# Optimization experiments

Measured on AMD Instinct MI355X. Metric: run time of the kernel, lower is better.

The kernel has to match this reference:

```python
import jax, jax.numpy as jnp
import numpy as np

C = 32          # d_model / channels
D_STATE = 32
D_CONV = 4
EXPAND = 2
D_INNER = EXPAND * C          # 64
DT_RANK = (C + 15) // 16      # ceil(32/16) = 2
EPS = 1e-5


def _conv2d(x, w, b):
    # x: (B,C,H,W), w: (O,I,3,3), stride 1, padding 1 (torch Conv2d)
    y = jax.lax.conv_general_dilated(
        x, w, window_strides=(1, 1), padding=[(1, 1), (1, 1)],
        dimension_numbers=("NCHW", "OIHW", "NCHW"))
    return y + b[None, :, None, None]


def _silu(x):
    return x * jax.nn.sigmoid(x)


def _mamba(xs, in_proj_w, conv1d_w, conv1d_b, x_proj_w, dt_proj_w, dt_proj_b,
           A_log, Dp, out_proj_w):
    # xs: (B, L, C)
    xz = xs @ in_proj_w.T                       # (B, L, 2*D_INNER)
    xm, z = jnp.split(xz, 2, axis=-1)           # each (B, L, D_INNER)

    # causal depthwise conv1d along L (torch: padding=d_conv-1 then [..., :L])
    xc = xm.transpose(0, 2, 1)                  # (B, D_INNER, L)
    xc = jax.lax.conv_general_dilated(
        xc, conv1d_w, window_strides=(1,), padding=[(D_CONV - 1, 0)],
        dimension_numbers=("NCH", "OIH", "NCH"),
        feature_group_count=D_INNER)
    xm = _silu((xc + conv1d_b[None, :, None]).transpose(0, 2, 1))  # (B,L,D_INNER)

    x_dbl = xm @ x_proj_w.T                     # (B, L, DT_RANK + 2*D_STATE)
    dt = x_dbl[..., :DT_RANK]
    Bm = x_dbl[..., DT_RANK:DT_RANK + D_STATE]  # (B, L, N)
    Cm = x_dbl[..., DT_RANK + D_STATE:]         # (B, L, N)

    delta = jax.nn.softplus(dt @ dt_proj_w.T + dt_proj_b)  # (B, L, D_INNER)
    A = -jnp.exp(A_log)                                     # (D_INNER, N)

    deltaA = jnp.exp(delta[..., None] * A)                           # (B,L,D,N)
    deltaBx = delta[..., None] * Bm[:, :, None, :] * xm[..., None]   # (B,L,D,N)

    def combine(c1, c2):
        a1, b1 = c1
        a2, b2 = c2
        return a1 * a2, a2 * b1 + b2

    # parallel linear recurrence h_t = deltaA_t * h_{t-1} + deltaBx_t
    _, hstate = jax.lax.associative_scan(combine, (deltaA, deltaBx), axis=1)

    y = jnp.einsum("bldn,bln->bld", hstate, Cm) + xm * Dp
    y = y * _silu(z)
    return y @ out_proj_w.T                     # (B, L, C)


def setup_inputs() -> dict:
    key = jax.random.key(0)
    ks = jax.random.split(key, 16)
    s = 0.02
    inp = {
        "x": jax.random.normal(ks[0], (4, C, 64, 64), dtype=jnp.float32),
        "conv1_w": jax.random.normal(ks[1], (2 * C, C, 3, 3), jnp.float32) * s,
        "conv1_b": jnp.zeros((2 * C,), jnp.float32),
        "conv2_w": jax.random.normal(ks[2], (C, 2 * C, 3, 3), jnp.float32) * s,
        "conv2_b": jnp.zeros((C,), jnp.float32),
        "ln_g": jnp.ones((C,), jnp.float32),
        "ln_b": jnp.zeros((C,), jnp.float32),
        "in_proj_w": jax.random.normal(ks[3], (2 * D_INNER, C), jnp.float32) * s,
        "conv1d_w": jax.random.normal(ks[4], (D_INNER, 1, D_CONV), jnp.float32) * 0.1,
        "conv1d_b": jnp.zeros((D_INNER,), jnp.float32),
        "x_proj_w": jax.random.normal(ks[5], (DT_RANK + 2 * D_STATE, D_INNER), jnp.float32) * s,
        "dt_proj_w": jax.random.normal(ks[6], (D_INNER, DT_RANK), jnp.float32) * 0.1,
        "dt_proj_b": jax.random.normal(ks[7], (D_INNER,), jnp.float32) * 0.1 - 4.0,
        "A_log": jnp.log(jnp.tile(jnp.arange(1, D_STATE + 1, dtype=jnp.float32), (D_INNER, 1))),
        "Dp": jnp.ones((D_INNER,), jnp.float32),
        "out_proj_w": jax.random.normal(ks[8], (C, D_INNER), jnp.float32) * s,
        "smooth_w": jax.random.normal(ks[9], (C, C, 3, 3), jnp.float32) * s,
        "smooth_b": jnp.zeros((C,), jnp.float32),
    }
    return inp


def reference(x, conv1_w, conv1_b, conv2_w, conv2_b, ln_g, ln_b,
              in_proj_w, conv1d_w, conv1d_b, x_proj_w, dt_proj_w, dt_proj_b,
              A_log, Dp, out_proj_w, smooth_w, smooth_b):
    b, c, h, w = x.shape
    # convb residual
    t = jax.nn.relu(_conv2d(x, conv1_w, conv1_b))
    x = _conv2d(t, conv2_w, conv2_b) + x
    # reshape (b,c,h,w) -> (b, h*w, c) row-major (faithful to torch .reshape)
    xs = x.reshape(b, -1, c)
    # LayerNorm over last dim
    mu = jnp.mean(xs, axis=-1, keepdims=True)
    var = jnp.mean(jnp.square(xs - mu), axis=-1, keepdims=True)
    xs = (xs - mu) * jax.lax.rsqrt(var + EPS) * ln_g + ln_b
    # Mamba block
    y = _mamba(xs, in_proj_w, conv1d_w, conv1d_b, x_proj_w, dt_proj_w,
               dt_proj_b, A_log, Dp, out_proj_w)
    y = y.transpose(0, 2, 1).reshape(b, c, h, w)
    return _conv2d(y, smooth_w, smooth_b)
```

## Files before the change

kernel.cpp:

```cpp
#include <hip/hip_runtime.h>
#include <math.h>

#define SEQL 4096
#define L2E 1.44269504088896340736f

#if defined(__has_builtin)
#if __has_builtin(__builtin_amdgcn_exp2f)
#define FAST_EXP2(x) __builtin_amdgcn_exp2f(x)
#endif
#endif
#ifndef FAST_EXP2
#define FAST_EXP2(x) exp2f(x)
#endif

__device__ __forceinline__ float sigmoid_f(float x){ return 1.0f/(1.0f+expf(-x)); }

template<int CI, int CO, int COG, bool RELU, bool RES>
__global__ __launch_bounds__(256) void conv3x3_k(const float* __restrict__ in,
    const float* __restrict__ wgt, const float* __restrict__ bias,
    const float* __restrict__ res, float* __restrict__ out)
{
  constexpr int CIT = CI/4;
  __shared__ float tin[4][2][6][72];
  __shared__ float red[3][4][COG][66];
  const int tid  = threadIdx.x;
  const int lane = tid & 63;
  const int ty   = tid >> 6;
  const int h0   = blockIdx.x * 4;
  const int co0  = blockIdx.y * COG;
  const int b    = blockIdx.z;

  if (lane < 24){
    int cl = lane / 12, rem = lane % 12, r = rem >> 1, side = rem & 1;
    tin[ty][cl][r][side ? 68 : 3] = 0.0f;
  }

  float acc[4][COG];
  #pragma unroll
  for (int rr=0;rr<4;++rr)
    #pragma unroll
    for (int u=0;u<COG;++u) acc[rr][u] = 0.0f;

  const int ci0 = ty*CIT;
  for (int cig = ci0; cig < ci0 + CIT; cig += 2){
    #pragma unroll
    for (int k=0;k<3;++k){
      int idx4 = lane + (k<<6);
      int row  = idx4 >> 4;
      int cl = row/6, r = row - cl*6;
      int w4 = (idx4 & 15) << 2;
      int h  = h0 - 1 + r;
      float4 v = make_float4(0.f,0.f,0.f,0.f);
      if (h>=0 && h<64)
        v = *(const float4*)(in + ((size_t)(b*CI+cig+cl)*64 + h)*64 + w4);
      *(float4*)&tin[ty][cl][r][4+w4] = v;
    }
    #pragma unroll
    for (int cl=0; cl<2; ++cl){
      float rv[6][3];
      #pragma unroll
      for (int r=0;r<6;++r)
        #pragma unroll
        for (int c=0;c<3;++c)
          rv[r][c] = tin[ty][cl][r][3+lane+c];
      #pragma unroll
      for (int u=0;u<COG;++u){
        const float* wp = wgt + ((size_t)(co0+u)*CI + cig + cl)*9;
        #pragma unroll
        for (int rr=0;rr<4;++rr)
          #pragma unroll
          for (int j=0;j<3;++j){
            acc[rr][u] = fmaf(rv[rr+j][0], wp[3*j+0], acc[rr][u]);
            acc[rr][u] = fmaf(rv[rr+j][1], wp[3*j+1], acc[rr][u]);
            acc[rr][u] = fmaf(rv[rr+j][2], wp[3*j+2], acc[rr][u]);
          }
      }
    }
  }
  if (ty > 0){
    #pragma unroll
    for (int rr=0;rr<4;++rr)
      #pragma unroll
      for (int u=0;u<COG;++u) red[ty-1][rr][u][lane] = acc[rr][u];
  }
  __syncthreads();
  if (ty == 0){
    #pragma unroll
    for (int rr=0;rr<4;++rr)
      #pragma unroll
      for (int u=0;u<COG;++u){
        float s = acc[rr][u] + red[0][rr][u][lane] + red[1][rr][u][lane]
                + red[2][rr][u][lane] + bias[co0+u];
        size_t ob = ((size_t)(b*CO+co0+u)*64 + h0+rr)*64 + lane;
        if constexpr (RES)  s += res[ob];
        if constexpr (RELU) s = fmaxf(s, 0.0f);
        out[ob] = s;
      }
  }
}

__global__ __launch_bounds__(1024, 4) void mamba_in_k(const float* __restrict__ x2,
    const float* __restrict__ g, const float* __restrict__ be,
    const float* __restrict__ Wip, const float* __restrict__ cw,
    const float* __restrict__ cb, const float* __restrict__ Wxp,
    const float* __restrict__ Wdt, const float* __restrict__ bdt,
    const float* __restrict__ A_log,
    float* __restrict__ xm2, float* __restrict__ szb, float* __restrict__ dlt,
    float* __restrict__ Bm, float* __restrict__ Cm,
    float* __restrict__ cA, float* __restrict__ cH)
{
  __shared__ __align__(16) float xn[68][37];
  __shared__ __align__(16) float xm[64][68];
  __shared__ __align__(16) float xtT[64][68];
  __shared__ __align__(16) float xd[64][67];
  float (*xbT)[68] = reinterpret_cast<float(*)[68]>(&xn[0][0]);
  const int tid = threadIdx.x, lane = tid & 63, ty = tid >> 6;
  const int bi = blockIdx.x >> 6;
  const int l0 = (blockIdx.x & 63) << 6;

  {
    const int row = tid >> 3, sub = tid & 7;
    if (row < 67){
      const int tok = l0 - 3 + row;
      const int c0 = sub << 2;
      if (tok >= 0){
        float4 f = *(const float4*)(x2 + (size_t)bi*131072 + (size_t)tok*32 + c0);
        float s = (f.x+f.y)+(f.z+f.w);
        s += __shfl_xor(s,1); s += __shfl_xor(s,2); s += __shfl_xor(s,4);
        const float mu = s * 0.03125f;
        float dx=f.x-mu, dy=f.y-mu, dz=f.z-mu, dw=f.w-mu;
        float q = (dx*dx+dy*dy)+(dz*dz+dw*dw);
        q += __shfl_xor(q,1); q += __shfl_xor(q,2); q += __shfl_xor(q,4);
        const float rstd = 1.0f/sqrtf(q*0.03125f + 1e-5f);
        xn[row][c0+0] = dx*rstd*g[c0+0] + be[c0+0];
        xn[row][c0+1] = dy*rstd*g[c0+1] + be[c0+1];
        xn[row][c0+2] = dz*rstd*g[c0+2] + be[c0+2];
        xn[row][c0+3] = dw*rstd*g[c0+3] + be[c0+3];
      } else {
        xn[row][c0+0]=0.0f; xn[row][c0+1]=0.0f;
        xn[row][c0+2]=0.0f; xn[row][c0+3]=0.0f;
      }
    }
  }
  __syncthreads();

  if (ty < 8){
    const int d0 = ty*8;
    float xvA[32];
    #pragma unroll
    for (int c=0;c<32;++c) xvA[c] = xn[lane][c];
    #pragma unroll
    for (int jj=0;jj<8;++jj){
      const float* wr = Wip + (d0+jj)*32;
      float a = 0.0f;
      #pragma unroll
      for (int c=0;c<32;++c) a = fmaf(xvA[c], wr[c], a);
      xm[d0+jj][lane] = a;
    }
    if (lane < 3){
      float xvB[32];
      #pragma unroll
      for (int c=0;c<32;++c) xvB[c] = xn[64+lane][c];
      #pragma unroll
      for (int jj=0;jj<8;++jj){
        const float* wr = Wip + (d0+jj)*32;
        float a = 0.0f;
        #pragma unroll
        for (int c=0;c<32;++c) a = fmaf(xvB[c], wr[c], a);
        xm[d0+jj][64+lane] = a;
      }
    }
  } else {
    const int d0z = (ty-8)*8;
    float xvC[32];
    #pragma unroll
    for (int c=0;c<32;++c) xvC[c] = xn[lane+3][c];
    #pragma unroll
    for (int jj=0;jj<8;++jj){
      const float* wr = Wip + (64+d0z+jj)*32;
      float a = 0.0f;
      #pragma unroll
      for (int c=0;c<32;++c) a = fmaf(xvC[c], wr[c], a);
      szb[((size_t)(bi*64+d0z+jj))*SEQL + l0 + lane] = a * sigmoid_f(a);
    }
  }
  __syncthreads();

  #pragma unroll
  for (int jj=0;jj<4;++jj){
    int d = ty*4 + jj;
    float a = xm[d][lane]*cw[d*4] + xm[d][lane+1]*cw[d*4+1]
            + xm[d][lane+2]*cw[d*4+2] + xm[d][lane+3]*cw[d*4+3] + cb[d];
    float s = a * sigmoid_f(a);
    xtT[d][lane] = s;
    xm2[((size_t)(bi*64+d))*SEQL + l0 + lane] = s;
  }
  __syncthreads();

  {
    float xv[64];
    #pragma unroll
    for (int c=0;c<64;++c) xv[c] = xtT[c][lane];
    for (int j=ty; j<66; j+=16){
      const float* wr = Wxp + j*64;
      float a = 0.0f;
      #pragma unroll
      for (int c=0;c<64;++c) a = fmaf(xv[c], wr[c], a);
      xd[lane][j] = a;
    }
  }
  __syncthreads();

  {
    float dt0 = xd[lane][0], dt1 = xd[lane][1];
    #pragma unroll
    for (int k=0;k<4;++k){
      int d2 = ty*4 + k;
      float v = dt0*Wdt[d2*2] + dt1*Wdt[d2*2+1] + bdt[d2];
      float sp = fmaxf(v,0.0f) + log1pf(expf(-fabsf(v)));
      dlt[((size_t)(bi*64+d2))*SEQL + l0 + lane] = sp;
      xm[d2][lane] = sp;
    }
    const int which = ty >> 3, gq = ty & 7;
    float* dst = which ? Cm : Bm;
    size_t base = ((size_t)bi*SEQL + l0 + lane)*32 + gq*4;
    const int s2 = 2 + which*32;
    float4 f0;
    f0.x = xd[lane][s2+gq+ 0]; f0.y = xd[lane][s2+gq+ 8];
    f0.z = xd[lane][s2+gq+16]; f0.w = xd[lane][s2+gq+24];
    *(float4*)(dst + base) = f0;
    if (!which){
      xbT[gq     ][lane] = f0.x;
      xbT[gq +  8][lane] = f0.y;
      xbT[gq + 16][lane] = f0.z;
      xbT[gq + 24][lane] = f0.w;
    }
  }
  __syncthreads();

  {
    const int d  = tid >> 4;
    const int gg = tid & 15;
    const int chunk = blockIdx.x & 63;
    const int bd = bi*64 + d;
    float Av0 = -expf(A_log[d*32 + gg     ]) * L2E;
    float Av1 = -expf(A_log[d*32 + gg + 16]) * L2E;
    float h0=0.0f, h1=0.0f, aP0=1.0f, aP1=1.0f;
    #pragma unroll 2
    for (int t0=0;t0<64;t0+=4){
      float4 dl4 = *(const float4*)&xm [d    ][t0];
      float4 xs4 = *(const float4*)&xtT[d    ][t0];
      float4 b04 = *(const float4*)&xbT[gg   ][t0];
      float4 b14 = *(const float4*)&xbT[gg+16][t0];
      #pragma unroll
      for (int k=0;k<4;++k){
        float dlv = (k==0)? dl4.x : (k==1)? dl4.y : (k==2)? dl4.z : dl4.w;
        float xsv = (k==0)? xs4.x : (k==1)? xs4.y : (k==2)? xs4.z : xs4.w;
        float bv0 = (k==0)? b04.x : (k==1)? b04.y : (k==2)? b04.z : b04.w;
        float bv1 = (k==0)? b14.x : (k==1)? b14.y : (k==2)? b14.z : b14.w;
        float m  = dlv * xsv;
        float a0 = FAST_EXP2(dlv*Av0);
        float a1 = FAST_EXP2(dlv*Av1);
        h0 = fmaf(a0, h0, m*bv0);  aP0 *= a0;
        h1 = fmaf(a1, h1, m*bv1);  aP1 *= a1;
      }
    }
    size_t idx0 = (((size_t)bd<<5) + gg     )*64 + chunk;
    size_t idx1 = (((size_t)bd<<5) + gg + 16)*64 + chunk;
    cA[idx0] = aP0; cH[idx0] = h0;
    cA[idx1] = aP1; cH[idx1] = h1;
  }
}

__global__ __launch_bounds__(256) void scan_p2(const float* __restrict__ dlt,
    const float* __restrict__ xssm, const float* __restrict__ Bm,
    const float* __restrict__ Cm, const float* __restrict__ A_log,
    const float* __restrict__ Dp, const float* __restrict__ sz,
    const float* __restrict__ cA, const float* __restrict__ cHs,
    float* __restrict__ yt)
{
  __shared__ float pre[32][34];
  const int tid = threadIdx.x;
  const int grp = blockIdx.x & 1;
  const int bd  = blockIdx.x >> 1;
  const int b = bd >> 6, d = bd & 63;
  const int c0 = grp << 5;

  if (tid < 32){
    const float* pa = cA  + (((size_t)bd<<5)+tid)*64;
    const float* ph = cHs + (((size_t)bd<<5)+tid)*64;
    float hrun = 0.0f;
    if (grp){
      #pragma unroll 4
      for (int c=0;c<32;c+=4){
        float4 a4 = *(const float4*)(pa+c);
        float4 h4 = *(const float4*)(ph+c);
        hrun = fmaf(a4.x,hrun,h4.x);
        hrun = fmaf(a4.y,hrun,h4.y);
        hrun = fmaf(a4.z,hrun,h4.z);
        hrun = fmaf(a4.w,hrun,h4.w);
      }
    }
    #pragma unroll 4
    for (int k=0;k<32;k+=4){
      float4 a4 = *(const float4*)(pa+c0+k);
      float4 h4 = *(const float4*)(ph+c0+k);
      pre[tid][k+0]=hrun; hrun=fmaf(a4.x,hrun,h4.x);
      pre[tid][k+1]=hrun; hrun=fmaf(a4.y,hrun,h4.y);
      pre[tid][k+2]=hrun; hrun=fmaf(a4.z,hrun,h4.z);
      pre[tid][k+3]=hrun; hrun=fmaf(a4.w,hrun,h4.w);
    }
  }
  __syncthreads();

  const int lc = tid >> 3, gg = tid & 7;
  const int chunk = c0 + lc;
  const int l0 = chunk << 6;
  const float Dv = Dp[d];
  float Av2[4], h[4];
  #pragma unroll
  for (int j=0;j<4;++j){
    Av2[j] = -expf(A_log[d*32 + gg + 8*j]) * L2E;
    h[j] = pre[gg + 8*j][lc];
  }
  const float* del = dlt  + (size_t)bd*SEQL + l0;
  const float* xp  = xssm + (size_t)bd*SEQL + l0;
  const float* szp = sz   + (size_t)bd*SEQL + l0;
  const float* Bp  = Bm + ((size_t)b*SEQL + l0)*32 + gg*4;
  const float* Cp  = Cm + ((size_t)b*SEQL + l0)*32 + gg*4;
  float* yp = yt + (size_t)bd*SEQL + l0;

  for (int i0=0;i0<64;i0+=16){
    float4 y4[4];
    #pragma unroll
    for (int s=0;s<4;++s){
      const int ib = i0 + s*4;
      float4 d4 = *(const float4*)(del+ib);
      float4 x4 = *(const float4*)(xp +ib);
      float4 s4 = *(const float4*)(szp+ib);
      #pragma unroll
      for (int t=0;t<4;++t){
        float dl = (t==0)? d4.x : (t==1)? d4.y : (t==2)? d4.z : d4.w;
        float xl = (t==0)? x4.x : (t==1)? x4.y : (t==2)? x4.z : x4.w;
        float sl = (t==0)? s4.x : (t==1)? s4.y : (t==2)? s4.z : s4.w;
        float4 bv = *(const float4*)(Bp + (ib+t)*32);
        float4 cv = *(const float4*)(Cp + (ib+t)*32);
        float a0 = FAST_EXP2(dl*Av2[0]); h[0] = fmaf(a0, h[0], dl*bv.x*xl);
        float a1 = FAST_EXP2(dl*Av2[1]); h[1] = fmaf(a1, h[1], dl*bv.y*xl);
        float a2 = FAST_EXP2(dl*Av2[2]); h[2] = fmaf(a2, h[2], dl*bv.z*xl);
        float a3 = FAST_EXP2(dl*Av2[3]); h[3] = fmaf(a3, h[3], dl*bv.w*xl);
        float v = fmaf(h[3], cv.w, fmaf(h[2], cv.z, fmaf(h[1], cv.y, h[0]*cv.x)));
        v += __shfl_xor(v,1); v += __shfl_xor(v,2); v += __shfl_xor(v,4);
        float yv = fmaf(xl, Dv, v) * sl;
        if      (t==0) y4[s].x = yv;
        else if (t==1) y4[s].y = yv;
        else if (t==2) y4[s].z = yv;
        else           y4[s].w = yv;
      }
    }
    if (gg < 4){
      float4 w = (gg==0) ? y4[0] : (gg==1) ? y4[1] : (gg==2) ? y4[2] : y4[3];
      *(float4*)(yp + i0 + gg*4) = w;
    }
  }
}

__global__ __launch_bounds__(512) void outproj_k(const float* __restrict__ yt,
    const float* __restrict__ Wout, float* __restrict__ ym)
{
  __shared__ float ys[64][67];
  const int tid = threadIdx.x, lane = tid & 63, ty = tid >> 6;
  const int bi = blockIdx.x >> 6;
  const int l0 = (blockIdx.x & 63) << 6;
  for (int r=ty; r<64; r+=8)
    ys[lane][r] = yt[((size_t)(bi*64+r))*SEQL + l0 + lane];
  __syncthreads();
  float yv[64];
  #pragma unroll
  for (int c=0;c<64;++c) yv[c] = ys[lane][c];
  #pragma unroll
  for (int jj=0;jj<4;++jj){
    int j = ty*4 + jj;
    const float* wr = Wout + j*64;
    float acc = 0.0f;
    #pragma unroll
    for (int c=0;c<64;++c) acc = fmaf(yv[c], wr[c], acc);
    ym[((size_t)(bi*32+j))*SEQL + l0 + lane] = acc;
  }
}

extern "C" void kernel_launch(void* const* d_in, const int* in_sizes, int n_in,
                              void* d_out, int out_size, void* d_ws, size_t ws_size,
                              hipStream_t stream) {
  const float* x        = (const float*)d_in[0];
  const float* conv1_w  = (const float*)d_in[1];
  const float* conv1_b  = (const float*)d_in[2];
  const float* conv2_w  = (const float*)d_in[3];
  const float* conv2_b  = (const float*)d_in[4];
  const float* ln_g     = (const float*)d_in[5];
  const float* ln_b     = (const float*)d_in[6];
  const float* in_proj_w= (const float*)d_in[7];
  const float* conv1d_w = (const float*)d_in[8];
  const float* conv1d_b = (const float*)d_in[9];
  const float* x_proj_w = (const float*)d_in[10];
  const float* dt_proj_w= (const float*)d_in[11];
  const float* dt_proj_b= (const float*)d_in[12];
  const float* A_log    = (const float*)d_in[13];
  const float* Dp       = (const float*)d_in[14];
  const float* out_proj_w=(const float*)d_in[15];
  const float* smooth_w = (const float*)d_in[16];
  const float* smooth_b = (const float*)d_in[17];
  float* out = (float*)d_out;

  float* ws = (float*)d_ws;
  float* t      = ws;
  float* x2     = t      + 1048576;
  float* xm2    = x2     + 524288;
  float* szb    = xm2    + 1048576;
  float* dlt    = szb    + 1048576;
  float* Bmat   = dlt    + 1048576;
  float* Cmat   = Bmat   + 524288;
  float* yt     = Cmat   + 524288;
  float* ym     = yt     + 1048576;
  float* cA     = t;
  float* cH     = t + 524288;

  conv3x3_k<32,64,4,true ,false><<<dim3(16,16,4), 256, 0, stream>>>(x,  conv1_w, conv1_b, nullptr, t);
  conv3x3_k<64,32,4,false,true ><<<dim3(16,8,4), 256, 0, stream>>>(t,  conv2_w, conv2_b, x,       x2);
  mamba_in_k  <<<256, 1024, 0, stream>>>(x2, ln_g, ln_b, in_proj_w, conv1d_w, conv1d_b,
                                         x_proj_w, dt_proj_w, dt_proj_b, A_log,
                                         xm2, szb, dlt, Bmat, Cmat, cA, cH);
  scan_p2     <<<512, 256, 0, stream>>>(dlt, xm2, Bmat, Cmat, A_log, Dp, szb, cA, cH, yt);
  outproj_k   <<<256, 512, 0, stream>>>(yt, out_proj_w, ym);
  conv3x3_k<32,32,4,false,false><<<dim3(16,8,4), 256, 0, stream>>>(ym, smooth_w, smooth_b, nullptr, out);
}
```

Before: 199.9 us.

## Make weight indices wave-uniform via readfirstlane and transpose chunk-state layout

Wraps the wave index in readfirstlane so weight addresses are provably uniform, letting the compiler use scalar (SMEM) loads for the projection weights. The weight reads are also turned into float4 loads. The chunk-state buffers cA/cH change from [bd][n][chunk] to [bd][chunk][n], so the chunk-scan writes become coalesced, while the prefix kernel now reads strided scalars instead of float4. The aim is to cut per-lane vector memory traffic for weights and scattered stores, at the risk of slower strided reads in the prefix kernel.

```diff
diff --git a/kernel.cpp b/kernel.cpp
--- a/kernel.cpp
+++ b/kernel.cpp
@@ -26,6 +26,7 @@
   const int tid  = threadIdx.x;
   const int lane = tid & 63;
   const int ty   = tid >> 6;
+  const int tyu  = __builtin_amdgcn_readfirstlane(ty);
   const int h0   = blockIdx.x * 4;
   const int co0  = blockIdx.y * COG;
   const int b    = blockIdx.z;
@@ -41,7 +42,7 @@
     #pragma unroll
     for (int u=0;u<COG;++u) acc[rr][u] = 0.0f;
 
-  const int ci0 = ty*CIT;
+  const int ci0 = tyu*CIT;
   for (int cig = ci0; cig < ci0 + CIT; cig += 2){
     #pragma unroll
     for (int k=0;k<3;++k){
@@ -115,6 +116,7 @@
   __shared__ __align__(16) float xd[64][67];
   float (*xbT)[68] = reinterpret_cast<float(*)[68]>(&xn[0][0]);
   const int tid = threadIdx.x, lane = tid & 63, ty = tid >> 6;
+  const int tyu = __builtin_amdgcn_readfirstlane(ty);
   const int bi = blockIdx.x >> 6;
   const int l0 = (blockIdx.x & 63) << 6;
 
@@ -132,10 +134,12 @@
         float q = (dx*dx+dy*dy)+(dz*dz+dw*dw);
         q += __shfl_xor(q,1); q += __shfl_xor(q,2); q += __shfl_xor(q,4);
         const float rstd = 1.0f/sqrtf(q*0.03125f + 1e-5f);
-        xn[row][c0+0] = dx*rstd*g[c0+0] + be[c0+0];
-        xn[row][c0+1] = dy*rstd*g[c0+1] + be[c0+1];
-        xn[row][c0+2] = dz*rstd*g[c0+2] + be[c0+2];
-        xn[row][c0+3] = dw*rstd*g[c0+3] + be[c0+3];
+        float4 gv = *(const float4*)(g  + c0);
+        float4 bv = *(const float4*)(be + c0);
+        xn[row][c0+0] = dx*rstd*gv.x + bv.x;
+        xn[row][c0+1] = dy*rstd*gv.y + bv.y;
+        xn[row][c0+2] = dz*rstd*gv.z + bv.z;
+        xn[row][c0+3] = dw*rstd*gv.w + bv.w;
       } else {
         xn[row][c0+0]=0.0f; xn[row][c0+1]=0.0f;
         xn[row][c0+2]=0.0f; xn[row][c0+3]=0.0f;
@@ -145,16 +149,22 @@
   __syncthreads();
 
   if (ty < 8){
-    const int d0 = ty*8;
+    const int d0 = tyu*8;
     float xvA[32];
     #pragma unroll
     for (int c=0;c<32;++c) xvA[c] = xn[lane][c];
     #pragma unroll
     for (int jj=0;jj<8;++jj){
-      const float* wr = Wip + (d0+jj)*32;
+      const float4* wr = (const float4*)(Wip + (d0+jj)*32);
       float a = 0.0f;
       #pragma unroll
-      for (int c=0;c<32;++c) a = fmaf(xvA[c], wr[c], a);
+      for (int c4=0;c4<8;++c4){
+        float4 w = wr[c4];
+        a = fmaf(xvA[c4*4+0], w.x, a);
+        a = fmaf(xvA[c4*4+1], w.y, a);
+        a = fmaf(xvA[c4*4+2], w.z, a);
+        a = fmaf(xvA[c4*4+3], w.w, a);
+      }
       xm[d0+jj][lane] = a;
     }
     if (lane < 3){
@@ -163,24 +173,36 @@
       for (int c=0;c<32;++c) xvB[c] = xn[64+lane][c];
       #pragma unroll
       for (int jj=0;jj<8;++jj){
-        const float* wr = Wip + (d0+jj)*32;
+        const float4* wr = (const float4*)(Wip + (d0+jj)*32);
         float a = 0.0f;
         #pragma unroll
-        for (int c=0;c<32;++c) a = fmaf(xvB[c], wr[c], a);
+        for (int c4=0;c4<8;++c4){
+          float4 w = wr[c4];
+          a = fmaf(xvB[c4*4+0], w.x, a);
+          a = fmaf(xvB[c4*4+1], w.y, a);
+          a = fmaf(xvB[c4*4+2], w.z, a);
+          a = fmaf(xvB[c4*4+3], w.w, a);
+        }
         xm[d0+jj][64+lane] = a;
       }
     }
   } else {
-    const int d0z = (ty-8)*8;
+    const int d0z = (tyu-8)*8;
     float xvC[32];
     #pragma unroll
     for (int c=0;c<32;++c) xvC[c] = xn[lane+3][c];
     #pragma unroll
     for (int jj=0;jj<8;++jj){
-      const float* wr = Wip + (64+d0z+jj)*32;
+      const float4* wr = (const float4*)(Wip + (64+d0z+jj)*32);
       float a = 0.0f;
       #pragma unroll
-      for (int c=0;c<32;++c) a = fmaf(xvC[c], wr[c], a);
+      for (int c4=0;c4<8;++c4){
+        float4 w = wr[c4];
+        a = fmaf(xvC[c4*4+0], w.x, a);
+        a = fmaf(xvC[c4*4+1], w.y, a);
+        a = fmaf(xvC[c4*4+2], w.z, a);
+        a = fmaf(xvC[c4*4+3], w.w, a);
+      }
       szb[((size_t)(bi*64+d0z+jj))*SEQL + l0 + lane] = a * sigmoid_f(a);
     }
   }
@@ -188,9 +210,10 @@
 
   #pragma unroll
   for (int jj=0;jj<4;++jj){
-    int d = ty*4 + jj;
-    float a = xm[d][lane]*cw[d*4] + xm[d][lane+1]*cw[d*4+1]
-            + xm[d][lane+2]*cw[d*4+2] + xm[d][lane+3]*cw[d*4+3] + cb[d];
+    int d = tyu*4 + jj;
+    float4 w = *(const float4*)(cw + d*4);
+    float a = xm[d][lane]*w.x + xm[d][lane+1]*w.y
+            + xm[d][lane+2]*w.z + xm[d][lane+3]*w.w + cb[d];
     float s = a * sigmoid_f(a);
     xtT[d][lane] = s;
     xm2[((size_t)(bi*64+d))*SEQL + l0 + lane] = s;
@@ -201,11 +224,17 @@
     float xv[64];
     #pragma unroll
     for (int c=0;c<64;++c) xv[c] = xtT[c][lane];
-    for (int j=ty; j<66; j+=16){
-      const float* wr = Wxp + j*64;
+    for (int j=tyu; j<66; j+=16){
+      const float4* wr = (const float4*)(Wxp + j*64);
       float a = 0.0f;
       #pragma unroll
-      for (int c=0;c<64;++c) a = fmaf(xv[c], wr[c], a);
+      for (int c4=0;c4<16;++c4){
+        float4 w = wr[c4];
+        a = fmaf(xv[c4*4+0], w.x, a);
+        a = fmaf(xv[c4*4+1], w.y, a);
+        a = fmaf(xv[c4*4+2], w.z, a);
+        a = fmaf(xv[c4*4+3], w.w, a);
+      }
       xd[lane][j] = a;
     }
   }
@@ -215,13 +244,14 @@
     float dt0 = xd[lane][0], dt1 = xd[lane][1];
     #pragma unroll
     for (int k=0;k<4;++k){
-      int d2 = ty*4 + k;
-      float v = dt0*Wdt[d2*2] + dt1*Wdt[d2*2+1] + bdt[d2];
+      int d2 = tyu*4 + k;
+      float2 wd = *(const float2*)(Wdt + d2*2);
+      float v = dt0*wd.x + dt1*wd.y + bdt[d2];
       float sp = fmaxf(v,0.0f) + log1pf(expf(-fabsf(v)));
       dlt[((size_t)(bi*64+d2))*SEQL + l0 + lane] = sp;
       xm[d2][lane] = sp;
     }
-    const int which = ty >> 3, gq = ty & 7;
+    const int which = tyu >> 3, gq = tyu & 7;
     float* dst = which ? Cm : Bm;
     size_t base = ((size_t)bi*SEQL + l0 + lane)*32 + gq*4;
     const int s2 = 2 + which*32;
@@ -265,10 +295,9 @@
         h1 = fmaf(a1, h1, m*bv1);  aP1 *= a1;
       }
     }
-    size_t idx0 = (((size_t)bd<<5) + gg     )*64 + chunk;
-    size_t idx1 = (((size_t)bd<<5) + gg + 16)*64 + chunk;
-    cA[idx0] = aP0; cH[idx0] = h0;
-    cA[idx1] = aP1; cH[idx1] = h1;
+    size_t base = ((size_t)bd*64 + chunk)*32;
+    cA[base + gg] = aP0; cA[base + gg + 16] = aP1;
+    cH[base + gg] = h0;  cH[base + gg + 16] = h1;
   }
 }
 
@@ -287,28 +316,18 @@
   const int c0 = grp << 5;
 
   if (tid < 32){
-    const float* pa = cA  + (((size_t)bd<<5)+tid)*64;
-    const float* ph = cHs + (((size_t)bd<<5)+tid)*64;
+    const float* pa = cA  + (size_t)bd*2048 + tid;
+    const float* ph = cHs + (size_t)bd*2048 + tid;
     float hrun = 0.0f;
     if (grp){
       #pragma unroll 4
-      for (int c=0;c<32;c+=4){
-        float4 a4 = *(const float4*)(pa+c);
-        float4 h4 = *(const float4*)(ph+c);
-        hrun = fmaf(a4.x,hrun,h4.x);
-        hrun = fmaf(a4.y,hrun,h4.y);
-        hrun = fmaf(a4.z,hrun,h4.z);
-        hrun = fmaf(a4.w,hrun,h4.w);
-      }
+      for (int c=0;c<32;++c)
+        hrun = fmaf(pa[c*32], hrun, ph[c*32]);
     }
     #pragma unroll 4
-    for (int k=0;k<32;k+=4){
-      float4 a4 = *(const float4*)(pa+c0+k);
-      float4 h4 = *(const float4*)(ph+c0+k);
-      pre[tid][k+0]=hrun; hrun=fmaf(a4.x,hrun,h4.x);
-      pre[tid][k+1]=hrun; hrun=fmaf(a4.y,hrun,h4.y);
-      pre[tid][k+2]=hrun; hrun=fmaf(a4.z,hrun,h4.z);
-      pre[tid][k+3]=hrun; hrun=fmaf(a4.w,hrun,h4.w);
+    for (int k=0;k<32;++k){
+      pre[tid][k] = hrun;
+      hrun = fmaf(pa[(c0+k)*32], hrun, ph[(c0+k)*32]);
     }
   }
   __syncthreads();
@@ -370,6 +389,7 @@
 {
   __shared__ float ys[64][67];
   const int tid = threadIdx.x, lane = tid & 63, ty = tid >> 6;
+  const int tyu = __builtin_amdgcn_readfirstlane(ty);
   const int bi = blockIdx.x >> 6;
   const int l0 = (blockIdx.x & 63) << 6;
   for (int r=ty; r<64; r+=8)
@@ -380,11 +400,17 @@
   for (int c=0;c<64;++c) yv[c] = ys[lane][c];
   #pragma unroll
   for (int jj=0;jj<4;++jj){
-    int j = ty*4 + jj;
-    const float* wr = Wout + j*64;
+    int j = tyu*4 + jj;
+    const float4* wr = (const float4*)(Wout + j*64);
     float acc = 0.0f;
     #pragma unroll
-    for (int c=0;c<64;++c) acc = fmaf(yv[c], wr[c], acc);
+    for (int c4=0;c4<16;++c4){
+      float4 w = wr[c4];
+      acc = fmaf(yv[c4*4+0], w.x, acc);
+      acc = fmaf(yv[c4*4+1], w.y, acc);
+      acc = fmaf(yv[c4*4+2], w.z, acc);
+      acc = fmaf(yv[c4*4+3], w.w, acc);
+    }
     ym[((size_t)(bi*32+j))*SEQL + l0 + lane] = acc;
   }
 }
```

New measurement: 192.1 us. 3.9% less time.
